# Performance work log

Measured on AMD Instinct MI355X. Metric: run time of the kernel, lower is better.

## Reference

```python
import jax, jax.numpy as jnp
import numpy as np

MARGIN = 1.0  # init kwarg 'margin'
NUM_CLASSES = 16


def setup_inputs() -> dict:
    key = jax.random.key(0)
    k1, k2 = jax.random.split(key)
    embeddings = jax.random.normal(k1, (384, 1024), dtype=jnp.float32)
    labels = jax.random.randint(k2, (384,), 0, NUM_CLASSES, dtype=jnp.int64)
    return {"embeddings": embeddings, "labels": labels}


def reference(embeddings, labels):
    # Dense, on-device equivalent of the CPU triplet mining:
    # valid triplet (a, p, n) iff labels[a]==labels[p], a<p, labels[n]!=labels[a].
    # Mean over all valid triplets == original torch losses.mean().
    B = embeddings.shape[0]
    sq = jnp.sum(embeddings * embeddings, axis=1)                      # [B]
    # Squared pairwise distances via Gram matrix (same math as (x_i-x_j)^2.sum())
    D = sq[:, None] + sq[None, :] - 2.0 * (embeddings @ embeddings.T)  # [B,B]

    eq = labels[:, None] == labels[None, :]                            # same-label mask [B,B]
    idx = jnp.arange(B)
    ap_valid = eq & (idx[:, None] < idx[None, :])                      # anchor<positive pairs
    mask = ap_valid[:, :, None] & (~eq)[:, None, :]                    # [a,p,n] valid triplets

    # loss[a,p,n] = relu(D[a,p] - D[a,n] + margin)
    loss = jax.nn.relu(D[:, :, None] - D[:, None, :] + MARGIN)         # [B,B,B]

    count = jnp.sum(mask)
    total = jnp.sum(jnp.where(mask, loss, jnp.float32(0.0)))
    mean = jnp.where(count > 0, total / count.astype(loss.dtype), jnp.float32(0.0))
    return mean, count
```

## Files before the change

kernel.cpp:

```cpp
#include <hip/hip_runtime.h>


constexpr int BN  = 384;
constexpr int DIM = 1024;
constexpr float MARGIN = 1.0f;
constexpr int LDK = 68;

__global__ __launch_bounds__(256) void gram_kernel(
    const float* __restrict__ E, float* __restrict__ P,
    float* __restrict__ sqpart, float* __restrict__ total,
    int* __restrict__ cnt, int* __restrict__ ticket, int KC, int NZ) {
    __shared__ float Ast[32 * LDK];
    __shared__ float Bst[32 * LDK];
    const int tx = threadIdx.x, ty = threadIdx.y;
    const int t  = ty * 16 + tx;
    const int i0 = blockIdx.y * 64, j0 = blockIdx.x * 64;
    const int z  = blockIdx.z;

    if (z == 0 && blockIdx.x == 0 && blockIdx.y == 0 && t == 0) {
        *total = 0.f; *cnt = 0; *ticket = 0;
    }

    const int r  = t >> 2;
    const int kq = t & 3;
    const int kb = kq * 8;
    const int rs = r ^ (kq << 4);

    const float* Ab = E + (size_t)(i0 + r) * DIM + z * KC + kb;
    const float* Bb = E + (size_t)(j0 + r) * DIM + z * KC + kb;

    float4 a0 = *(const float4*)(Ab);
    float4 a1 = *(const float4*)(Ab + 4);
    float4 b0 = *(const float4*)(Bb);
    float4 b1 = *(const float4*)(Bb + 4);

    float acc[4][4] = {};

    for (int kt = 0; kt < KC; kt += 32) {
        Ast[(kb + 0) * LDK + rs] = a0.x; Ast[(kb + 1) * LDK + rs] = a0.y;
        Ast[(kb + 2) * LDK + rs] = a0.z; Ast[(kb + 3) * LDK + rs] = a0.w;
        Ast[(kb + 4) * LDK + rs] = a1.x; Ast[(kb + 5) * LDK + rs] = a1.y;
        Ast[(kb + 6) * LDK + rs] = a1.z; Ast[(kb + 7) * LDK + rs] = a1.w;
        Bst[(kb + 0) * LDK + rs] = b0.x; Bst[(kb + 1) * LDK + rs] = b0.y;
        Bst[(kb + 2) * LDK + rs] = b0.z; Bst[(kb + 3) * LDK + rs] = b0.w;
        Bst[(kb + 4) * LDK + rs] = b1.x; Bst[(kb + 5) * LDK + rs] = b1.y;
        Bst[(kb + 6) * LDK + rs] = b1.z; Bst[(kb + 7) * LDK + rs] = b1.w;
        __syncthreads();
        if (kt + 32 < KC) {
            a0 = *(const float4*)(Ab + kt + 32);
            a1 = *(const float4*)(Ab + kt + 36);
            b0 = *(const float4*)(Bb + kt + 32);
            b1 = *(const float4*)(Bb + kt + 36);
        }
#pragma unroll
        for (int kk = 0; kk < 32; ++kk) {
            const int sw = (kk >> 3) << 4;
            const float4 av = *(const float4*)&Ast[kk * LDK + ((4 * ty) ^ sw)];
            const float4 bv = *(const float4*)&Bst[kk * LDK + ((4 * tx) ^ sw)];
            const float aa[4] = {av.x, av.y, av.z, av.w};
            const float bb[4] = {bv.x, bv.y, bv.z, bv.w};
#pragma unroll
            for (int i2 = 0; i2 < 4; ++i2)
#pragma unroll
                for (int j2 = 0; j2 < 4; ++j2)
                    acc[i2][j2] += aa[i2] * bb[j2];
        }
        __syncthreads();
    }

    const size_t rowstride = (size_t)NZ * BN;
#pragma unroll
    for (int i2 = 0; i2 < 4; ++i2) {
        const float4 w = make_float4(acc[i2][0], acc[i2][1], acc[i2][2], acc[i2][3]);
        *(float4*)&P[(size_t)(i0 + 4 * ty + i2) * rowstride + (size_t)z * BN + (j0 + 4 * tx)] = w;
    }
    if (blockIdx.x == blockIdx.y && tx == ty) {
#pragma unroll
        for (int i2 = 0; i2 < 4; ++i2)
            sqpart[z * BN + (i0 + 4 * ty + i2)] = acc[i2][i2];
    }
}

template <int NZ>
__global__ __launch_bounds__(128) void triplet_kernel(
    const float* __restrict__ P, const float* __restrict__ sqpart,
    const int* __restrict__ labels, float* __restrict__ total,
    int* __restrict__ cnt, int* __restrict__ ticket, float* __restrict__ out) {
    __shared__ float Hrow[BN];
    __shared__ int   lab[BN];
    __shared__ int   poslist[BN];
    __shared__ int   npos_s;
    __shared__ float wsum[2];
    __shared__ int   wcnt[2];
    const int a   = blockIdx.x;
    const int tid = threadIdx.x;

    if (tid == 0) npos_s = 0;
    for (int i = tid; i < BN; i += 128) lab[i] = labels[i];

    if (tid < 96) {
        const int c0 = tid * 4;
        float4 g = make_float4(0.f, 0.f, 0.f, 0.f);
        float4 s = make_float4(0.f, 0.f, 0.f, 0.f);
#pragma unroll
        for (int z = 0; z < NZ; ++z) {
            const float4 pv = *(const float4*)&P[(size_t)a * ((size_t)NZ * BN) + z * BN + c0];
            const float4 sv = *(const float4*)&sqpart[z * BN + c0];
            g.x += pv.x; g.y += pv.y; g.z += pv.z; g.w += pv.w;
            s.x += sv.x; s.y += sv.y; s.z += sv.z; s.w += sv.w;
        }
        Hrow[c0 + 0] = s.x - 2.f * g.x;
        Hrow[c0 + 1] = s.y - 2.f * g.y;
        Hrow[c0 + 2] = s.z - 2.f * g.z;
        Hrow[c0 + 3] = s.w - 2.f * g.w;
    }
    __syncthreads();

    const int la = lab[a];
    int lc = 0;
#pragma unroll
    for (int q = 0; q < 3; ++q) {
        const int p = tid + q * 128;
        if (lab[p] != la) ++lc;
        else if (p > a) { const int k = atomicAdd(&npos_s, 1); poslist[k] = p; }
    }
    __syncthreads();
    const int np = npos_s;

    const float hn0 = Hrow[tid];
    const float hn1 = Hrow[tid + 128];
    const float hn2 = Hrow[tid + 256];
    const bool  ng0 = (lab[tid]       != la);
    const bool  ng1 = (lab[tid + 128] != la);
    const bool  ng2 = (lab[tid + 256] != la);

    float ls = 0.f;
    for (int k = 0; k < np; ++k) {
        const float dpm = Hrow[poslist[k]] + MARGIN;
        if (ng0) { const float v = dpm - hn0; ls += (v > 0.f) ? v : 0.f; }
        if (ng1) { const float v = dpm - hn1; ls += (v > 0.f) ? v : 0.f; }
        if (ng2) { const float v = dpm - hn2; ls += (v > 0.f) ? v : 0.f; }
    }

#pragma unroll
    for (int off = 32; off; off >>= 1) {
        ls += __shfl_down(ls, off);
        lc += __shfl_down(lc, off);
    }
    const int wave = tid >> 6, lane = tid & 63;
    if (lane == 0) { wsum[wave] = ls; wcnt[wave] = lc; }
    __syncthreads();
    if (tid == 0) {
        const float s    = wsum[0] + wsum[1];
        const int   nneg = wcnt[0] + wcnt[1];
        if (s != 0.f) atomicAdd(total, s);
        if (np)       atomicAdd(cnt, np * nneg);
        __threadfence();
        const int done = atomicAdd(ticket, 1);
        if (done == (int)gridDim.x - 1) {
            const float tot = atomicAdd(total, 0.0f);
            const int   c   = atomicAdd(cnt, 0);
            out[0] = (c > 0) ? tot / (float)c : 0.f;
            out[1] = (float)c;
        }
    }
}

extern "C" void kernel_launch(void* const* d_in, const int* in_sizes, int n_in,
                              void* d_out, int out_size, void* d_ws, size_t ws_size,
                              hipStream_t stream) {
    const float* E      = (const float*)d_in[0];
    const int*   labels = (const int*)d_in[1];
    float*       out    = (float*)d_out;

    int Z = 1;
    for (int cand : {16, 8, 4, 2}) {
        size_t need = (size_t)cand * BN * BN * 4 + (size_t)cand * BN * 4 + 64;
        if (need <= ws_size) { Z = cand; break; }
    }

    char*  ws     = (char*)d_ws;
    float* P      = (float*)ws;
    float* sqpart = (float*)(ws + (size_t)Z * BN * BN * 4);
    float* total  = (float*)(ws + (size_t)Z * BN * BN * 4 + (size_t)Z * BN * 4);
    int*   cnt    = (int*)(total + 1);
    int*   ticket = (int*)(total + 2);

    gram_kernel<<<dim3(6, 6, Z), dim3(16, 16), 0, stream>>>(
        E, P, sqpart, total, cnt, ticket, DIM / Z, Z);

    switch (Z) {
        case 16: triplet_kernel<16><<<BN, 128, 0, stream>>>(P, sqpart, labels, total, cnt, ticket, out); break;
        case 8:  triplet_kernel<8> <<<BN, 128, 0, stream>>>(P, sqpart, labels, total, cnt, ticket, out); break;
        case 4:  triplet_kernel<4> <<<BN, 128, 0, stream>>>(P, sqpart, labels, total, cnt, ticket, out); break;
        case 2:  triplet_kernel<2> <<<BN, 128, 0, stream>>>(P, sqpart, labels, total, cnt, ticket, out); break;
        default: triplet_kernel<1> <<<BN, 128, 0, stream>>>(P, sqpart, labels, total, cnt, ticket, out); break;
    }
}
```

Before: 82.33 us.

## Use 128x128 symmetric Gram tiles with 8x8 per-thread blocking and deeper split-K

The Gram kernel now computes only the upper-triangular 128x128 tiles (6 per K-slice) and writes each off-diagonal tile twice, transposed, exploiting symmetry to halve FLOPs. Per-thread accumulators grow from 4x4 to 8x8 for more register reuse per shared-memory load, and split-K can go up to 32 slices to keep enough blocks in flight. Register prefetch of the next K chunk is dropped in favour of loading at the start of each iteration. The triplet kernel has to sum more partial slices, and the higher register use may cut occupancy.

Result: slower. 90.88 us (+10.4%).

```diff
diff --git a/kernel.cpp b/kernel.cpp
--- a/kernel.cpp
+++ b/kernel.cpp
@@ -4,80 +4,98 @@
 constexpr int BN  = 384;
 constexpr int DIM = 1024;
 constexpr float MARGIN = 1.0f;
-constexpr int LDK = 68;
+constexpr int LDST = 140;
 
 __global__ __launch_bounds__(256) void gram_kernel(
     const float* __restrict__ E, float* __restrict__ P,
     float* __restrict__ sqpart, float* __restrict__ total,
     int* __restrict__ cnt, int* __restrict__ ticket, int KC, int NZ) {
-    __shared__ float Ast[32 * LDK];
-    __shared__ float Bst[32 * LDK];
-    const int tx = threadIdx.x, ty = threadIdx.y;
-    const int t  = ty * 16 + tx;
-    const int i0 = blockIdx.y * 64, j0 = blockIdx.x * 64;
-    const int z  = blockIdx.z;
-
-    if (z == 0 && blockIdx.x == 0 && blockIdx.y == 0 && t == 0) {
-        *total = 0.f; *cnt = 0; *ticket = 0;
-    }
-
-    const int r  = t >> 2;
-    const int kq = t & 3;
-    const int kb = kq * 8;
-    const int rs = r ^ (kq << 4);
-
-    const float* Ab = E + (size_t)(i0 + r) * DIM + z * KC + kb;
-    const float* Bb = E + (size_t)(j0 + r) * DIM + z * KC + kb;
-
-    float4 a0 = *(const float4*)(Ab);
-    float4 a1 = *(const float4*)(Ab + 4);
-    float4 b0 = *(const float4*)(Bb);
-    float4 b1 = *(const float4*)(Bb + 4);
-
-    float acc[4][4] = {};
+    __shared__ float Ast[32 * LDST];
+    __shared__ float Bst[32 * LDST];
+    const int t    = threadIdx.x;
+    const int tile = blockIdx.x % 6;
+    const int z    = blockIdx.x / 6;
+    const int ti   = (tile < 3) ? 0 : ((tile < 5) ? 1 : 2);
+    const int tj   = (tile < 3) ? tile : ((tile < 5) ? tile - 2 : 2);
+    const int i0   = ti * 128, j0 = tj * 128;
+
+    if (blockIdx.x == 0 && t == 0) { *total = 0.f; *cnt = 0; *ticket = 0; }
+
+    const int r  = t >> 1;
+    const int h  = t & 1;
+    const int pr = r + 4 * (r >> 5);
+    const float* Ab = E + (size_t)(i0 + r) * DIM + (size_t)z * KC + h * 16;
+    const float* Bb = E + (size_t)(j0 + r) * DIM + (size_t)z * KC + h * 16;
+
+    const int tx = t & 15, ty = t >> 4;
+    const int pa = 8 * ty + 4 * (ty >> 2);
+    const int pb = 8 * tx + 4 * (tx >> 2);
+
+    float acc[8][8] = {};
 
     for (int kt = 0; kt < KC; kt += 32) {
-        Ast[(kb + 0) * LDK + rs] = a0.x; Ast[(kb + 1) * LDK + rs] = a0.y;
-        Ast[(kb + 2) * LDK + rs] = a0.z; Ast[(kb + 3) * LDK + rs] = a0.w;
-        Ast[(kb + 4) * LDK + rs] = a1.x; Ast[(kb + 5) * LDK + rs] = a1.y;
-        Ast[(kb + 6) * LDK + rs] = a1.z; Ast[(kb + 7) * LDK + rs] = a1.w;
-        Bst[(kb + 0) * LDK + rs] = b0.x; Bst[(kb + 1) * LDK + rs] = b0.y;
-        Bst[(kb + 2) * LDK + rs] = b0.z; Bst[(kb + 3) * LDK + rs] = b0.w;
-        Bst[(kb + 4) * LDK + rs] = b1.x; Bst[(kb + 5) * LDK + rs] = b1.y;
-        Bst[(kb + 6) * LDK + rs] = b1.z; Bst[(kb + 7) * LDK + rs] = b1.w;
+        float4 av0 = *(const float4*)(Ab + kt);
+        float4 av1 = *(const float4*)(Ab + kt + 4);
+        float4 av2 = *(const float4*)(Ab + kt + 8);
+        float4 av3 = *(const float4*)(Ab + kt + 12);
+        float4 bv0 = *(const float4*)(Bb + kt);
+        float4 bv1 = *(const float4*)(Bb + kt + 4);
+        float4 bv2 = *(const float4*)(Bb + kt + 8);
+        float4 bv3 = *(const float4*)(Bb + kt + 12);
+        if (kt) __syncthreads();
+        const int kb = 16 * h;
+        Ast[(kb + 0)  * LDST + pr] = av0.x; Ast[(kb + 1)  * LDST + pr] = av0.y;
+        Ast[(kb + 2)  * LDST + pr] = av0.z; Ast[(kb + 3)  * LDST + pr] = av0.w;
+        Ast[(kb + 4)  * LDST + pr] = av1.x; Ast[(kb + 5)  * LDST + pr] = av1.y;
+        Ast[(kb + 6)  * LDST + pr] = av1.z; Ast[(kb + 7)  * LDST + pr] = av1.w;
+        Ast[(kb + 8)  * LDST + pr] = av2.x; Ast[(kb + 9)  * LDST + pr] = av2.y;
+        Ast[(kb + 10) * LDST + pr] = av2.z; Ast[(kb + 11) * LDST + pr] = av2.w;
+        Ast[(kb + 12) * LDST + pr] = av3.x; Ast[(kb + 13) * LDST + pr] = av3.y;
+        Ast[(kb + 14) * LDST + pr] = av3.z; Ast[(kb + 15) * LDST + pr] = av3.w;
+        Bst[(kb + 0)  * LDST + pr] = bv0.x; Bst[(kb + 1)  * LDST + pr] = bv0.y;
+        Bst[(kb + 2)  * LDST + pr] = bv0.z; Bst[(kb + 3)  * LDST + pr] = bv0.w;
+        Bst[(kb + 4)  * LDST + pr] = bv1.x; Bst[(kb + 5)  * LDST + pr] = bv1.y;
+        Bst[(kb + 6)  * LDST + pr] = bv1.z; Bst[(kb + 7)  * LDST + pr] = bv1.w;
+        Bst[(kb + 8)  * LDST + pr] = bv2.x; Bst[(kb + 9)  * LDST + pr] = bv2.y;
+        Bst[(kb + 10) * LDST + pr] = bv2.z; Bst[(kb + 11) * LDST + pr] = bv2.w;
+        Bst[(kb + 12) * LDST + pr] = bv3.x; Bst[(kb + 13) * LDST + pr] = bv3.y;
+        Bst[(kb + 14) * LDST + pr] = bv3.z; Bst[(kb + 15) * LDST + pr] = bv3.w;
         __syncthreads();
-        if (kt + 32 < KC) {
-            a0 = *(const float4*)(Ab + kt + 32);
-            a1 = *(const float4*)(Ab + kt + 36);
-            b0 = *(const float4*)(Bb + kt + 32);
-            b1 = *(const float4*)(Bb + kt + 36);
-        }
 #pragma unroll
         for (int kk = 0; kk < 32; ++kk) {
-            const int sw = (kk >> 3) << 4;
-            const float4 av = *(const float4*)&Ast[kk * LDK + ((4 * ty) ^ sw)];
-            const float4 bv = *(const float4*)&Bst[kk * LDK + ((4 * tx) ^ sw)];
-            const float aa[4] = {av.x, av.y, av.z, av.w};
-            const float bb[4] = {bv.x, bv.y, bv.z, bv.w};
-#pragma unroll
-            for (int i2 = 0; i2 < 4; ++i2)
-#pragma unroll
-                for (int j2 = 0; j2 < 4; ++j2)
+            const float4 a0 = *(const float4*)&Ast[kk * LDST + pa];
+            const float4 a1 = *(const float4*)&Ast[kk * LDST + pa + 4];
+            const float4 b0 = *(const float4*)&Bst[kk * LDST + pb];
+            const float4 b1 = *(const float4*)&Bst[kk * LDST + pb + 4];
+            const float aa[8] = {a0.x, a0.y, a0.z, a0.w, a1.x, a1.y, a1.z, a1.w};
+            const float bb[8] = {b0.x, b0.y, b0.z, b0.w, b1.x, b1.y, b1.z, b1.w};
+#pragma unroll
+            for (int i2 = 0; i2 < 8; ++i2)
+#pragma unroll
+                for (int j2 = 0; j2 < 8; ++j2)
                     acc[i2][j2] += aa[i2] * bb[j2];
         }
-        __syncthreads();
-    }
-
-    const size_t rowstride = (size_t)NZ * BN;
-#pragma unroll
-    for (int i2 = 0; i2 < 4; ++i2) {
-        const float4 w = make_float4(acc[i2][0], acc[i2][1], acc[i2][2], acc[i2][3]);
-        *(float4*)&P[(size_t)(i0 + 4 * ty + i2) * rowstride + (size_t)z * BN + (j0 + 4 * tx)] = w;
-    }
-    if (blockIdx.x == blockIdx.y && tx == ty) {
-#pragma unroll
-        for (int i2 = 0; i2 < 4; ++i2)
-            sqpart[z * BN + (i0 + 4 * ty + i2)] = acc[i2][i2];
+    }
+
+    const size_t ZBN = (size_t)NZ * BN;
+    const int row0 = i0 + 8 * ty, col0 = j0 + 8 * tx;
+#pragma unroll
+    for (int i2 = 0; i2 < 8; ++i2) {
+        float* dst = &P[(size_t)(row0 + i2) * ZBN + (size_t)z * BN + col0];
+        *(float4*)(dst)     = make_float4(acc[i2][0], acc[i2][1], acc[i2][2], acc[i2][3]);
+        *(float4*)(dst + 4) = make_float4(acc[i2][4], acc[i2][5], acc[i2][6], acc[i2][7]);
+    }
+    if (ti != tj) {
+#pragma unroll
+        for (int j2 = 0; j2 < 8; ++j2) {
+            float* dst = &P[(size_t)(col0 + j2) * ZBN + (size_t)z * BN + row0];
+            *(float4*)(dst)     = make_float4(acc[0][j2], acc[1][j2], acc[2][j2], acc[3][j2]);
+            *(float4*)(dst + 4) = make_float4(acc[4][j2], acc[5][j2], acc[6][j2], acc[7][j2]);
+        }
+    } else if (tx == ty) {
+#pragma unroll
+        for (int i2 = 0; i2 < 8; ++i2)
+            sqpart[z * BN + row0 + i2] = acc[i2][i2];
     }
 }
 
@@ -174,7 +192,7 @@
     float*       out    = (float*)d_out;
 
     int Z = 1;
-    for (int cand : {16, 8, 4, 2}) {
+    for (int cand : {32, 16, 8, 4, 2}) {
         size_t need = (size_t)cand * BN * BN * 4 + (size_t)cand * BN * 4 + 64;
         if (need <= ws_size) { Z = cand; break; }
     }
@@ -186,10 +204,10 @@
     int*   cnt    = (int*)(total + 1);
     int*   ticket = (int*)(total + 2);
 
-    gram_kernel<<<dim3(6, 6, Z), dim3(16, 16), 0, stream>>>(
-        E, P, sqpart, total, cnt, ticket, DIM / Z, Z);
+    gram_kernel<<<6 * Z, 256, 0, stream>>>(E, P, sqpart, total, cnt, ticket, DIM / Z, Z);
 
     switch (Z) {
+        case 32: triplet_kernel<32><<<BN, 128, 0, stream>>>(P, sqpart, labels, total, cnt, ticket, out); break;
         case 16: triplet_kernel<16><<<BN, 128, 0, stream>>>(P, sqpart, labels, total, cnt, ticket, out); break;
         case 8:  triplet_kernel<8> <<<BN, 128, 0, stream>>>(P, sqpart, labels, total, cnt, ticket, out); break;
         case 4:  triplet_kernel<4> <<<BN, 128, 0, stream>>>(P, sqpart, labels, total, cnt, ticket, out); break;
```
